# Performance work log

Hardware: AMD Instinct MI355X
Metric: run time of the kernel (lower is better)

Reference implementation:

```python
import jax, jax.numpy as jnp
import numpy as np

EMBED_DIM = 768
NUM_HEADS = 12
HEAD_DIM = EMBED_DIM // NUM_HEADS


def setup_inputs() -> dict:
    key = jax.random.key(0)
    ks = jax.random.split(key, 9)
    B, N, D = 8, 1024, EMBED_DIM
    s = 1.0 / np.sqrt(D)
    x = jax.random.normal(ks[0], (B, N, D), dtype=jnp.float32)
    Wq = jax.random.normal(ks[1], (D, D), dtype=jnp.float32) * s
    bq = jnp.zeros((D,), dtype=jnp.float32)
    Wk = jax.random.normal(ks[2], (D, D), dtype=jnp.float32) * s
    bk = jnp.zeros((D,), dtype=jnp.float32)
    Wv = jax.random.normal(ks[3], (D, D), dtype=jnp.float32) * s
    bv = jnp.zeros((D,), dtype=jnp.float32)
    Wo = jax.random.normal(ks[4], (D, D), dtype=jnp.float32) * s
    bo = jnp.zeros((D,), dtype=jnp.float32)
    return {"x": x, "Wq": Wq, "bq": bq, "Wk": Wk, "bk": bk,
            "Wv": Wv, "bv": bv, "Wo": Wo, "bo": bo}


def reference(x, Wq, bq, Wk, bk, Wv, bv, Wo, bo):
    B, N, D = x.shape
    H, Hd = NUM_HEADS, HEAD_DIM
    # torch Linear: y = x @ W.T + b
    q = (x @ Wq.T + bq).reshape(B, N, H, Hd).transpose(0, 2, 1, 3)  # [B,H,N,Hd]
    k = (x @ Wk.T + bk).reshape(B, N, H, Hd).transpose(0, 2, 1, 3)
    v = (x @ Wv.T + bv).reshape(B, N, H, Hd).transpose(0, 2, 1, 3)
    # NOTE: original scales by embed_dim**-0.5 (not head_dim)
    scale = jnp.asarray(D, x.dtype) ** -0.5
    scores = jnp.einsum('bhnd,bhmd->bhnm', q, k) * scale  # [B,H,N,N]
    attn = jax.nn.softmax(scores, axis=-1)
    out = jnp.einsum('bhnm,bhmd->bhnd', attn, v)  # dropout: identity in eval
    out = out.transpose(0, 2, 1, 3).reshape(B, N, D)
    return out @ Wo.T + bo
```

## Files before the change

### kernel.cpp

```cpp
#include <hip/hip_runtime.h>
#include <math.h>


typedef __bf16 bf16x8 __attribute__((ext_vector_type(8)));
typedef float  f32x4  __attribute__((ext_vector_type(4)));
typedef unsigned u32x2 __attribute__((ext_vector_type(2)));
typedef unsigned u32x4 __attribute__((ext_vector_type(4)));
typedef unsigned short ushort_t;

__device__ __forceinline__ unsigned short f2bf(float f) {
    unsigned u = __float_as_uint(f);
    u += 0x7fffu + ((u >> 16) & 1u);
    return (unsigned short)(u >> 16);
}
__device__ __forceinline__ unsigned pk16(unsigned short lo, unsigned short hi) {
    return (unsigned)lo | ((unsigned)hi << 16);
}

#define GLL16(g, l)                                                                        \
    __builtin_amdgcn_global_load_lds((const __attribute__((address_space(1))) void*)(g),   \
                                     (__attribute__((address_space(3))) void*)(l), 16, 0, 0)

__global__ __launch_bounds__(256)
void cast_all(const float* __restrict__ x,
              const float* __restrict__ w0, const float* __restrict__ w1,
              const float* __restrict__ w2, const float* __restrict__ w3,
              ushort_t* __restrict__ xb, ushort_t* __restrict__ wb0,
              ushort_t* __restrict__ wb1, ushort_t* __restrict__ wb2,
              ushort_t* __restrict__ wb3)
{
    const int y = blockIdx.y;
    const float* s; ushort_t* d; int n;
    switch (y) {
        case 0:  s = x;  d = xb;  n = 8192 * 768; break;
        case 1:  s = w0; d = wb0; n = 768 * 768;  break;
        case 2:  s = w1; d = wb1; n = 768 * 768;  break;
        case 3:  s = w2; d = wb2; n = 768 * 768;  break;
        default: s = w3; d = wb3; n = 768 * 768;  break;
    }
    const int i = (blockIdx.x * 256 + threadIdx.x) * 8;
    if (i >= n) return;
    const float4 f0 = *(const float4*)(s + i);
    const float4 f1 = *(const float4*)(s + i + 4);
    ushort4 p0, p1;
    p0.x = f2bf(f0.x); p0.y = f2bf(f0.y); p0.z = f2bf(f0.z); p0.w = f2bf(f0.w);
    p1.x = f2bf(f1.x); p1.y = f2bf(f1.y); p1.z = f2bf(f1.z); p1.w = f2bf(f1.w);
    *(ushort4*)(d + i)     = p0;
    *(ushort4*)(d + i + 4) = p1;
}

__device__ __forceinline__ void gemm_core_mfma(
    const ushort_t* __restrict__ A, const ushort_t* __restrict__ W,
    int m0, int n0, ushort_t* smem, f32x4 acc[4][4])
{
    ushort_t* As = smem;
    ushort_t* Ws = smem + 4096;
    const int tid = threadIdx.x;
    const int L   = tid & 63;
    const int wv  = tid >> 6;
    const int wr  = wv >> 1, wc = wv & 1;
    const int c   = L & 15,  g  = L >> 4;

    const int c0 = tid, c1 = tid + 256;
    const ushort_t* a0 = A + (size_t)(m0 + (c0 >> 2)) * 768 + (c0 & 3) * 8;
    const ushort_t* a1 = A + (size_t)(m0 + (c1 >> 2)) * 768 + (c1 & 3) * 8;
    const ushort_t* w0 = W + (size_t)(n0 + (c0 >> 2)) * 768 + (c0 & 3) * 8;
    const ushort_t* w1 = W + (size_t)(n0 + (c1 >> 2)) * 768 + (c1 & 3) * 8;

#pragma unroll
    for (int i = 0; i < 4; ++i)
#pragma unroll
        for (int j = 0; j < 4; ++j) acc[i][j] = (f32x4){0.f, 0.f, 0.f, 0.f};

    for (int k0 = 0; k0 < 768; k0 += 32) {
        __syncthreads();
        GLL16(a0 + k0, &As[(size_t)c0 * 8]);
        GLL16(a1 + k0, &As[(size_t)c1 * 8]);
        GLL16(w0 + k0, &Ws[(size_t)c0 * 8]);
        GLL16(w1 + k0, &Ws[(size_t)c1 * 8]);
        __syncthreads();
        bf16x8 af[4], bfr[4];
#pragma unroll
        for (int i = 0; i < 4; ++i)
            af[i] = *(const bf16x8*)&As[(wr * 64 + i * 16 + c) * 32 + g * 8];
#pragma unroll
        for (int j = 0; j < 4; ++j)
            bfr[j] = *(const bf16x8*)&Ws[(wc * 64 + j * 16 + c) * 32 + g * 8];
#pragma unroll
        for (int i = 0; i < 4; ++i)
#pragma unroll
            for (int j = 0; j < 4; ++j)
                acc[i][j] = __builtin_amdgcn_mfma_f32_16x16x32_bf16(
                    af[i], bfr[j], acc[i][j], 0, 0, 0);
    }
}

__global__ __launch_bounds__(256, 2)
void gemm_qkv(const ushort_t* __restrict__ xb,
              const ushort_t* __restrict__ wqb, const ushort_t* __restrict__ wkb,
              const ushort_t* __restrict__ wvb,
              const float* __restrict__ bq, const float* __restrict__ bk,
              const float* __restrict__ bv,
              ushort_t* __restrict__ Qh, ushort_t* __restrict__ Kl,
              ushort_t* __restrict__ Vl)
{
    __shared__ ushort_t smem[8192];
    const int z = blockIdx.z;
    const ushort_t* W   = (z == 0) ? wqb : (z == 1) ? wkb : wvb;
    const float*    bia = (z == 0) ? bq  : (z == 1) ? bk  : bv;
    const int m0 = blockIdx.y * 128, n0 = blockIdx.x * 128;
    f32x4 acc[4][4];
    gemm_core_mfma(xb, W, m0, n0, smem, acc);

    const int tid = threadIdx.x, L = tid & 63, wv2 = tid >> 6;
    const int wr = wv2 >> 1, wc = wv2 & 1, c = L & 15, g = L >> 4;
    ushort_t* scr = smem + wv2 * 1280;
    const int h = (n0 + wc * 64) >> 6;
    float bsv[4];
#pragma unroll
    for (int j = 0; j < 4; ++j) bsv[j] = bia[n0 + wc * 64 + j * 16 + c];

    __syncthreads();
#pragma unroll
    for (int i = 0; i < 4; ++i) {
        const int rowg = m0 + wr * 64 + i * 16;
        const int b  = rowg >> 10;
        const int nb = rowg & 1023;
        const int bh = b * 12 + h;
        if (z < 2) {
#pragma unroll
            for (int j = 0; j < 4; ++j)
#pragma unroll
                for (int r = 0; r < 4; ++r)
                    scr[(g * 4 + r) * 72 + j * 16 + c] = f2bf(acc[i][j][r] + bsv[j]);
            if (z == 0) {
                const int row = L >> 2, qp = L & 3;
                const u32x4 v0 = *(const u32x4*)&scr[row * 72 + qp * 16];
                const u32x4 v1 = *(const u32x4*)&scr[row * 72 + qp * 16 + 8];
                ushort_t* dst = Qh + ((size_t)bh * 1024 + nb + row) * 64 + qp * 16;
                *(u32x4*)dst       = v0;
                *(u32x4*)(dst + 8) = v1;
            } else {
                const int n16 = L >> 2, q1 = L & 3;
                const u32x4 va = *(const u32x4*)&scr[n16 * 72 + q1 * 8];
                const u32x4 vb2 = *(const u32x4*)&scr[n16 * 72 + q1 * 8 + 32];
                ushort_t* base = Kl + (size_t)bh * 65536 + (size_t)(nb >> 4) * 1024;
                *(u32x4*)&base[q1 * 128 + n16 * 8]       = va;
                *(u32x4*)&base[512 + q1 * 128 + n16 * 8] = vb2;
            }
        } else {
#pragma unroll
            for (int j = 0; j < 4; ++j) {
                const unsigned w01 = pk16(f2bf(acc[i][j][0] + bsv[j]),
                                          f2bf(acc[i][j][1] + bsv[j]));
                const unsigned w23 = pk16(f2bf(acc[i][j][2] + bsv[j]),
                                          f2bf(acc[i][j][3] + bsv[j]));
                const int a = (j * 16 + c) * 20 + g * 4;
                *(unsigned*)&scr[a]     = w01;
                *(unsigned*)&scr[a + 2] = w23;
            }
            const u32x2 r0 = *(const u32x2*)&scr[L * 20];
            const u32x2 r1 = *(const u32x2*)&scr[L * 20 + 4];
            const u32x2 r2 = *(const u32x2*)&scr[L * 20 + 8];
            const u32x2 r3 = *(const u32x2*)&scr[L * 20 + 12];
            const int ht = L >> 4, cV = L & 15;
            const int T = nb >> 6, u = (nb >> 5) & 1, gVa = (nb >> 3) & 3;
            ushort_t* vb = Vl + (((size_t)(bh * 4 + ht) * 16 + T) * 2 + u) * 512 + cV * 8;
            *(u32x4*)&vb[gVa * 128]       = (u32x4){r0.x, r0.y, r1.x, r1.y};
            *(u32x4*)&vb[(gVa + 1) * 128] = (u32x4){r2.x, r2.y, r3.x, r3.y};
        }
    }
}

__global__ __launch_bounds__(256, 2)
void gemm_outp(const ushort_t* __restrict__ attnb, const ushort_t* __restrict__ wob,
               const float* __restrict__ bo, float* __restrict__ out)
{
    __shared__ ushort_t smem[8192];
    const int m0 = blockIdx.y * 128, n0 = blockIdx.x * 128;
    f32x4 acc[4][4];
    gemm_core_mfma(attnb, wob, m0, n0, smem, acc);
    const int tid = threadIdx.x, L = tid & 63, wv2 = tid >> 6;
    const int wr = wv2 >> 1, wc = wv2 & 1, c = L & 15, g = L >> 4;
#pragma unroll
    for (int i = 0; i < 4; ++i) {
        const int row = m0 + wr * 64 + i * 16 + g * 4;
#pragma unroll
        for (int j = 0; j < 4; ++j) {
            const int col = n0 + wc * 64 + j * 16 + c;
            const float bsvo = bo[col];
#pragma unroll
            for (int r = 0; r < 4; ++r)
                out[(size_t)(row + r) * 768 + col] = acc[i][j][r] + bsvo;
        }
    }
}

__global__ __launch_bounds__(128, 4)
void flash_bf16(const ushort_t* __restrict__ Q, const ushort_t* __restrict__ Kl,
                const ushort_t* __restrict__ Vl, ushort_t* __restrict__ attnb)
{
    __shared__ ushort_t Ps[2][2][16 * 68];
    __shared__ f32x4 Comb[64 * 9];
    const int tid = threadIdx.x;
    const int wv = tid >> 6, L = tid & 63, c = L & 15, g = L >> 4;
    const int bh = blockIdx.y, q0 = blockIdx.x * 32;
    const float SC2 = 0.05205954985329743f;

    const ushort_t* Qp = Q + ((size_t)bh * 1024 + q0 + c) * 64 + g * 8;
    bf16x8 qf[2][2];
    qf[0][0] = *(const bf16x8*)Qp;
    qf[0][1] = *(const bf16x8*)(Qp + 32);
    qf[1][0] = *(const bf16x8*)(Qp + 1024);
    qf[1][1] = *(const bf16x8*)(Qp + 1056);

    const ushort_t* Kb = Kl + (size_t)bh * 65536 + (size_t)L * 8;
    const ushort_t* Vb = Vl + (size_t)bh * 65536 + (size_t)L * 8;

    f32x4 o[2][4];
#pragma unroll
    for (int w = 0; w < 2; ++w)
#pragma unroll
        for (int ht = 0; ht < 4; ++ht) o[w][ht] = (f32x4){0.f, 0.f, 0.f, 0.f};
    float ls[2] = {0.f, 0.f};

    const int Tbeg = wv * 8;
    for (int T = Tbeg; T < Tbeg + 8; ++T) {
        bf16x8 kf0[4], kf1[4];
#pragma unroll
        for (int ct = 0; ct < 4; ++ct) {
            const ushort_t* kp = Kb + (size_t)((T * 4 + ct) * 2) * 512;
            kf0[ct] = *(const bf16x8*)kp;
            kf1[ct] = *(const bf16x8*)(kp + 512);
        }
#pragma unroll
        for (int w = 0; w < 2; ++w) {
            f32x4 s[4];
#pragma unroll
            for (int ct = 0; ct < 4; ++ct) {
                f32x4 zz = (f32x4){0.f, 0.f, 0.f, 0.f};
                zz = __builtin_amdgcn_mfma_f32_16x16x32_bf16(kf0[ct], qf[w][0], zz, 0, 0, 0);
                zz = __builtin_amdgcn_mfma_f32_16x16x32_bf16(kf1[ct], qf[w][1], zz, 0, 0, 0);
                s[ct] = zz;
            }
#pragma unroll
            for (int ct = 0; ct < 4; ++ct) {
                float p[4];
#pragma unroll
                for (int r = 0; r < 4; ++r) p[r] = exp2f(s[ct][r] * SC2);
                const unsigned w01 = __builtin_amdgcn_perm(
                    __float_as_uint(p[1]), __float_as_uint(p[0]), 0x07060302u);
                const unsigned w23 = __builtin_amdgcn_perm(
                    __float_as_uint(p[3]), __float_as_uint(p[2]), 0x07060302u);
                ls[w] += __uint_as_float(w01 << 16) + __uint_as_float(w01 & 0xffff0000u)
                       + __uint_as_float(w23 << 16) + __uint_as_float(w23 & 0xffff0000u);
                *(u32x2*)&Ps[wv][w][c * 68 + ct * 16 + g * 4] = (u32x2){w01, w23};
            }
        }
        const int pb = c * 68 + g * 8;
        bf16x8 pf[2][2];
#pragma unroll
        for (int w = 0; w < 2; ++w) {
            pf[w][0] = __builtin_bit_cast(bf16x8, *(const u32x4*)&Ps[wv][w][pb]);
            pf[w][1] = __builtin_bit_cast(bf16x8, *(const u32x4*)&Ps[wv][w][pb + 32]);
        }
#pragma unroll
        for (int ht = 0; ht < 4; ++ht) {
            const ushort_t* vp = Vb + (size_t)((ht * 16 + T) * 2) * 512;
            const bf16x8 v0 = *(const bf16x8*)vp;
            const bf16x8 v1 = *(const bf16x8*)(vp + 512);
#pragma unroll
            for (int w = 0; w < 2; ++w) {
                o[w][ht] = __builtin_amdgcn_mfma_f32_16x16x32_bf16(v0, pf[w][0], o[w][ht], 0, 0, 0);
                o[w][ht] = __builtin_amdgcn_mfma_f32_16x16x32_bf16(v1, pf[w][1], o[w][ht], 0, 0, 0);
            }
        }
    }

    if (wv == 1) {
#pragma unroll
        for (int w = 0; w < 2; ++w)
#pragma unroll
            for (int ht = 0; ht < 4; ++ht) Comb[L * 9 + w * 4 + ht] = o[w][ht];
        Comb[L * 9 + 8] = (f32x4){ls[0], ls[1], 0.f, 0.f};
    }
    __syncthreads();
    if (wv == 0) {
#pragma unroll
        for (int w = 0; w < 2; ++w)
#pragma unroll
            for (int ht = 0; ht < 4; ++ht) o[w][ht] += Comb[L * 9 + w * 4 + ht];
        const f32x4 lw = Comb[L * 9 + 8];
        ls[0] += lw.x;
        ls[1] += lw.y;

        const int b = bh / 12, h = bh % 12;
#pragma unroll
        for (int w = 0; w < 2; ++w) {
            float l = ls[w];
            l += __shfl_xor(l, 16);
            l += __shfl_xor(l, 32);
            const float inv = 1.f / l;
#pragma unroll
            for (int ht = 0; ht < 4; ++ht) {
                const unsigned w0 = pk16(f2bf(o[w][ht][0] * inv), f2bf(o[w][ht][1] * inv));
                const unsigned w1 = pk16(f2bf(o[w][ht][2] * inv), f2bf(o[w][ht][3] * inv));
                *(u32x2*)&Ps[0][w][c * 68 + ht * 16 + g * 4] = (u32x2){w0, w1};
            }
#pragma unroll
            for (int e = 0; e < 2; ++e) {
                const int row = e * 8 + (L >> 3);
                const int ch  = L & 7;
                const int si  = row * 68 + ch * 8;
                const u32x2 t0 = *(const u32x2*)&Ps[0][w][si];
                const u32x2 t1 = *(const u32x2*)&Ps[0][w][si + 4];
                *(u32x4*)&attnb[((size_t)(b * 1024 + q0 + w * 16 + row)) * 768 + h * 64 + ch * 8]
                    = (u32x4){t0.x, t0.y, t1.x, t1.y};
            }
        }
    }
}

extern "C" void kernel_launch(void* const* d_in, const int* in_sizes, int n_in,
                              void* d_out, int out_size, void* d_ws, size_t ws_size,
                              hipStream_t stream)
{
    const float* x  = (const float*)d_in[0];
    const float* Wq = (const float*)d_in[1];
    const float* bq = (const float*)d_in[2];
    const float* Wk = (const float*)d_in[3];
    const float* bk = (const float*)d_in[4];
    const float* Wv = (const float*)d_in[5];
    const float* bv = (const float*)d_in[6];
    const float* Wo = (const float*)d_in[7];
    const float* bo = (const float*)d_in[8];
    float* out = (float*)d_out;

    char* ws = (char*)d_ws;
    ushort_t* xb    = (ushort_t*)(ws);
    ushort_t* wqb   = (ushort_t*)(ws + 12582912);
    ushort_t* wkb   = (ushort_t*)(ws + 12582912 + 1179648);
    ushort_t* wvb   = (ushort_t*)(ws + 12582912 + 2359296);
    ushort_t* wob   = (ushort_t*)(ws + 12582912 + 3538944);
    ushort_t* Qh    = (ushort_t*)(ws + 17301504);
    ushort_t* Kl    = (ushort_t*)(ws + 29884416);
    ushort_t* Vl    = (ushort_t*)(ws + 42467328);
    ushort_t* attnb = (ushort_t*)(ws + 55050240);

    cast_all<<<dim3(3072, 5), 256, 0, stream>>>(x, Wq, Wk, Wv, Wo,
                                                xb, wqb, wkb, wvb, wob);
    gemm_qkv<<<dim3(6, 64, 3), 256, 0, stream>>>(xb, wqb, wkb, wvb,
                                                 bq, bk, bv, Qh, Kl, Vl);
    flash_bf16<<<dim3(32, 96), 128, 0, stream>>>(Qh, Kl, Vl, attnb);
    gemm_outp<<<dim3(6, 64), 256, 0, stream>>>(attnb, wob, bo, out);
}
```

Measured before the change: 219.1 us.

## Swizzle GEMM LDS tiles, prefetch K/V in flash loop, split epilogue across waves

The GEMM core now XOR-swizzles the 16-byte chunk placement in LDS so that the bf16x8 fragment reads avoid bank conflicts. In the flash kernel, the K fragments for the next tile are loaded during the current tile's compute and the V fragments are loaded at the top of each iteration, so global latency is hidden behind the MFMAs. exp2f is replaced by the hardware exp2 intrinsic, and the row sum now accumulates unrounded fp32 values instead of bf16-rounded ones. The final combine is split so each wave normalises and writes one of the two query groups, using a union to share LDS. Occupancy hints change: GEMMs go to 3 blocks and flash to 3 blocks, which trades registers against prefetch buffers.

```diff
diff --git a/kernel.cpp b/kernel.cpp
--- a/kernel.cpp
+++ b/kernel.cpp
@@ -62,10 +62,12 @@
     const int c   = L & 15,  g  = L >> 4;
 
     const int c0 = tid, c1 = tid + 256;
-    const ushort_t* a0 = A + (size_t)(m0 + (c0 >> 2)) * 768 + (c0 & 3) * 8;
-    const ushort_t* a1 = A + (size_t)(m0 + (c1 >> 2)) * 768 + (c1 & 3) * 8;
-    const ushort_t* w0 = W + (size_t)(n0 + (c0 >> 2)) * 768 + (c0 & 3) * 8;
-    const ushort_t* w1 = W + (size_t)(n0 + (c1 >> 2)) * 768 + (c1 & 3) * 8;
+    const int qs = ((tid & 3) ^ ((tid >> 3) & 3)) * 8;
+    const ushort_t* a0 = A + (size_t)(m0 + (c0 >> 2)) * 768 + qs;
+    const ushort_t* a1 = A + (size_t)(m0 + (c1 >> 2)) * 768 + qs;
+    const ushort_t* w0 = W + (size_t)(n0 + (c0 >> 2)) * 768 + qs;
+    const ushort_t* w1 = W + (size_t)(n0 + (c1 >> 2)) * 768 + qs;
+    const int sg = (g ^ ((c >> 1) & 3)) * 8;
 
 #pragma unroll
     for (int i = 0; i < 4; ++i)
@@ -82,10 +84,10 @@
         bf16x8 af[4], bfr[4];
 #pragma unroll
         for (int i = 0; i < 4; ++i)
-            af[i] = *(const bf16x8*)&As[(wr * 64 + i * 16 + c) * 32 + g * 8];
+            af[i] = *(const bf16x8*)&As[(wr * 64 + i * 16 + c) * 32 + sg];
 #pragma unroll
         for (int j = 0; j < 4; ++j)
-            bfr[j] = *(const bf16x8*)&Ws[(wc * 64 + j * 16 + c) * 32 + g * 8];
+            bfr[j] = *(const bf16x8*)&Ws[(wc * 64 + j * 16 + c) * 32 + sg];
 #pragma unroll
         for (int i = 0; i < 4; ++i)
 #pragma unroll
@@ -95,7 +97,7 @@
     }
 }
 
-__global__ __launch_bounds__(256, 2)
+__global__ __launch_bounds__(256, 3)
 void gemm_qkv(const ushort_t* __restrict__ xb,
               const ushort_t* __restrict__ wqb, const ushort_t* __restrict__ wkb,
               const ushort_t* __restrict__ wvb,
@@ -142,7 +144,7 @@
                 *(u32x4*)(dst + 8) = v1;
             } else {
                 const int n16 = L >> 2, q1 = L & 3;
-                const u32x4 va = *(const u32x4*)&scr[n16 * 72 + q1 * 8];
+                const u32x4 va  = *(const u32x4*)&scr[n16 * 72 + q1 * 8];
                 const u32x4 vb2 = *(const u32x4*)&scr[n16 * 72 + q1 * 8 + 32];
                 ushort_t* base = Kl + (size_t)bh * 65536 + (size_t)(nb >> 4) * 1024;
                 *(u32x4*)&base[q1 * 128 + n16 * 8]       = va;
@@ -172,7 +174,7 @@
     }
 }
 
-__global__ __launch_bounds__(256, 2)
+__global__ __launch_bounds__(256, 3)
 void gemm_outp(const ushort_t* __restrict__ attnb, const ushort_t* __restrict__ wob,
                const float* __restrict__ bo, float* __restrict__ out)
 {
@@ -196,12 +198,16 @@
     }
 }
 
-__global__ __launch_bounds__(128, 4)
+union FlashSmem {
+    ushort_t ps[2][2][16 * 68];
+    f32x4 comb[2][64 * 5];
+};
+
+__global__ __launch_bounds__(128, 3)
 void flash_bf16(const ushort_t* __restrict__ Q, const ushort_t* __restrict__ Kl,
                 const ushort_t* __restrict__ Vl, ushort_t* __restrict__ attnb)
 {
-    __shared__ ushort_t Ps[2][2][16 * 68];
-    __shared__ f32x4 Comb[64 * 9];
+    __shared__ FlashSmem sm;
     const int tid = threadIdx.x;
     const int wv = tid >> 6, L = tid & 63, c = L & 15, g = L >> 4;
     const int bh = blockIdx.y, q0 = blockIdx.x * 32;
@@ -224,100 +230,103 @@
         for (int ht = 0; ht < 4; ++ht) o[w][ht] = (f32x4){0.f, 0.f, 0.f, 0.f};
     float ls[2] = {0.f, 0.f};
 
-    const int Tbeg = wv * 8;
-    for (int T = Tbeg; T < Tbeg + 8; ++T) {
-        bf16x8 kf0[4], kf1[4];
-#pragma unroll
-        for (int ct = 0; ct < 4; ++ct) {
-            const ushort_t* kp = Kb + (size_t)((T * 4 + ct) * 2) * 512;
-            kf0[ct] = *(const bf16x8*)kp;
-            kf1[ct] = *(const bf16x8*)(kp + 512);
-        }
-#pragma unroll
-        for (int w = 0; w < 2; ++w) {
-            f32x4 s[4];
+    const int Tbeg = wv * 8, Tend = Tbeg + 8;
+
+    bf16x8 kf0[4], kf1[4];
+#pragma unroll
+    for (int ct = 0; ct < 4; ++ct) {
+        const ushort_t* kp = Kb + (size_t)((Tbeg * 4 + ct) * 2) * 512;
+        kf0[ct] = *(const bf16x8*)kp;
+        kf1[ct] = *(const bf16x8*)(kp + 512);
+    }
+
+    for (int T = Tbeg; T < Tend; ++T) {
+        bf16x8 vf0[4], vf1[4];
+#pragma unroll
+        for (int ht = 0; ht < 4; ++ht) {
+            const ushort_t* vp = Vb + (size_t)((ht * 16 + T) * 2) * 512;
+            vf0[ht] = *(const bf16x8*)vp;
+            vf1[ht] = *(const bf16x8*)(vp + 512);
+        }
+        f32x4 s[2][4];
+#pragma unroll
+        for (int w = 0; w < 2; ++w)
 #pragma unroll
             for (int ct = 0; ct < 4; ++ct) {
                 f32x4 zz = (f32x4){0.f, 0.f, 0.f, 0.f};
                 zz = __builtin_amdgcn_mfma_f32_16x16x32_bf16(kf0[ct], qf[w][0], zz, 0, 0, 0);
                 zz = __builtin_amdgcn_mfma_f32_16x16x32_bf16(kf1[ct], qf[w][1], zz, 0, 0, 0);
-                s[ct] = zz;
-            }
+                s[w][ct] = zz;
+            }
+        const int Tn = (T + 1 < Tend) ? T + 1 : T;
+#pragma unroll
+        for (int ct = 0; ct < 4; ++ct) {
+            const ushort_t* kp = Kb + (size_t)((Tn * 4 + ct) * 2) * 512;
+            kf0[ct] = *(const bf16x8*)kp;
+            kf1[ct] = *(const bf16x8*)(kp + 512);
+        }
+#pragma unroll
+        for (int w = 0; w < 2; ++w) {
 #pragma unroll
             for (int ct = 0; ct < 4; ++ct) {
                 float p[4];
 #pragma unroll
-                for (int r = 0; r < 4; ++r) p[r] = exp2f(s[ct][r] * SC2);
+                for (int r = 0; r < 4; ++r)
+                    p[r] = __builtin_amdgcn_exp2f(s[w][ct][r] * SC2);
+                ls[w] += (p[0] + p[1]) + (p[2] + p[3]);
                 const unsigned w01 = __builtin_amdgcn_perm(
                     __float_as_uint(p[1]), __float_as_uint(p[0]), 0x07060302u);
                 const unsigned w23 = __builtin_amdgcn_perm(
                     __float_as_uint(p[3]), __float_as_uint(p[2]), 0x07060302u);
-                ls[w] += __uint_as_float(w01 << 16) + __uint_as_float(w01 & 0xffff0000u)
-                       + __uint_as_float(w23 << 16) + __uint_as_float(w23 & 0xffff0000u);
-                *(u32x2*)&Ps[wv][w][c * 68 + ct * 16 + g * 4] = (u32x2){w01, w23};
+                *(u32x2*)&sm.ps[wv][w][c * 68 + ct * 16 + g * 4] = (u32x2){w01, w23};
             }
         }
         const int pb = c * 68 + g * 8;
-        bf16x8 pf[2][2];
 #pragma unroll
         for (int w = 0; w < 2; ++w) {
-            pf[w][0] = __builtin_bit_cast(bf16x8, *(const u32x4*)&Ps[wv][w][pb]);
-            pf[w][1] = __builtin_bit_cast(bf16x8, *(const u32x4*)&Ps[wv][w][pb + 32]);
-        }
-#pragma unroll
-        for (int ht = 0; ht < 4; ++ht) {
-            const ushort_t* vp = Vb + (size_t)((ht * 16 + T) * 2) * 512;
-            const bf16x8 v0 = *(const bf16x8*)vp;
-            const bf16x8 v1 = *(const bf16x8*)(vp + 512);
-#pragma unroll
-            for (int w = 0; w < 2; ++w) {
-                o[w][ht] = __builtin_amdgcn_mfma_f32_16x16x32_bf16(v0, pf[w][0], o[w][ht], 0, 0, 0);
-                o[w][ht] = __builtin_amdgcn_mfma_f32_16x16x32_bf16(v1, pf[w][1], o[w][ht], 0, 0, 0);
-            }
-        }
-    }
-
-    if (wv == 1) {
-#pragma unroll
-        for (int w = 0; w < 2; ++w)
-#pragma unroll
-            for (int ht = 0; ht < 4; ++ht) Comb[L * 9 + w * 4 + ht] = o[w][ht];
-        Comb[L * 9 + 8] = (f32x4){ls[0], ls[1], 0.f, 0.f};
-    }
+            const bf16x8 pf0 = __builtin_bit_cast(bf16x8, *(const u32x4*)&sm.ps[wv][w][pb]);
+            const bf16x8 pf1 = __builtin_bit_cast(bf16x8, *(const u32x4*)&sm.ps[wv][w][pb + 32]);
+#pragma unroll
+            for (int ht = 0; ht < 4; ++ht) {
+                o[w][ht] = __builtin_amdgcn_mfma_f32_16x16x32_bf16(vf0[ht], pf0, o[w][ht], 0, 0, 0);
+                o[w][ht] = __builtin_amdgcn_mfma_f32_16x16x32_bf16(vf1[ht], pf1, o[w][ht], 0, 0, 0);
+            }
+        }
+    }
+
     __syncthreads();
-    if (wv == 0) {
-#pragma unroll
-        for (int w = 0; w < 2; ++w)
-#pragma unroll
-            for (int ht = 0; ht < 4; ++ht) o[w][ht] += Comb[L * 9 + w * 4 + ht];
-        const f32x4 lw = Comb[L * 9 + 8];
-        ls[0] += lw.x;
-        ls[1] += lw.y;
-
-        const int b = bh / 12, h = bh % 12;
-#pragma unroll
-        for (int w = 0; w < 2; ++w) {
-            float l = ls[w];
-            l += __shfl_xor(l, 16);
-            l += __shfl_xor(l, 32);
-            const float inv = 1.f / l;
-#pragma unroll
-            for (int ht = 0; ht < 4; ++ht) {
-                const unsigned w0 = pk16(f2bf(o[w][ht][0] * inv), f2bf(o[w][ht][1] * inv));
-                const unsigned w1 = pk16(f2bf(o[w][ht][2] * inv), f2bf(o[w][ht][3] * inv));
-                *(u32x2*)&Ps[0][w][c * 68 + ht * 16 + g * 4] = (u32x2){w0, w1};
-            }
-#pragma unroll
-            for (int e = 0; e < 2; ++e) {
-                const int row = e * 8 + (L >> 3);
-                const int ch  = L & 7;
-                const int si  = row * 68 + ch * 8;
-                const u32x2 t0 = *(const u32x2*)&Ps[0][w][si];
-                const u32x2 t1 = *(const u32x2*)&Ps[0][w][si + 4];
-                *(u32x4*)&attnb[((size_t)(b * 1024 + q0 + w * 16 + row)) * 768 + h * 64 + ch * 8]
-                    = (u32x4){t0.x, t0.y, t1.x, t1.y};
-            }
-        }
+
+    const int other = wv ^ 1;
+#pragma unroll
+    for (int ht = 0; ht < 4; ++ht) sm.comb[other][L * 5 + ht] = o[other][ht];
+    sm.comb[other][L * 5 + 4] = (f32x4){ls[other], 0.f, 0.f, 0.f};
+    __syncthreads();
+
+    f32x4 oc[4];
+#pragma unroll
+    for (int ht = 0; ht < 4; ++ht) oc[ht] = o[wv][ht] + sm.comb[wv][L * 5 + ht];
+    float lc = ls[wv] + sm.comb[wv][L * 5 + 4].x;
+    lc += __shfl_xor(lc, 16);
+    lc += __shfl_xor(lc, 32);
+    const float inv = 1.f / lc;
+
+    ushort_t* strip = (ushort_t*)&sm.comb[wv][0];
+#pragma unroll
+    for (int ht = 0; ht < 4; ++ht) {
+        const unsigned w0 = pk16(f2bf(oc[ht][0] * inv), f2bf(oc[ht][1] * inv));
+        const unsigned w1 = pk16(f2bf(oc[ht][2] * inv), f2bf(oc[ht][3] * inv));
+        *(u32x2*)&strip[c * 68 + ht * 16 + g * 4] = (u32x2){w0, w1};
+    }
+    const int b = bh / 12, h = bh % 12;
+#pragma unroll
+    for (int e = 0; e < 2; ++e) {
+        const int row = e * 8 + (L >> 3);
+        const int ch  = L & 7;
+        const int si  = row * 68 + ch * 8;
+        const u32x2 t0 = *(const u32x2*)&strip[si];
+        const u32x2 t1 = *(const u32x2*)&strip[si + 4];
+        *(u32x4*)&attnb[((size_t)(b * 1024 + q0 + wv * 16 + row)) * 768 + h * 64 + ch * 8]
+            = (u32x4){t0.x, t0.y, t1.x, t1.y};
     }
 }
 
```

New measurement: 222.3 us. About the same (+1.5%).
